# Kernel optimization log

Measured on AMD Instinct MI355X. Metric: run time of the kernel, lower is better.

## Reference

```python
import jax, jax.numpy as jnp
import numpy as np

B, S, D = 4, 2048, 1024  # batch, seq (== context_size), d_in == d_out


def setup_inputs() -> dict:
    key = jax.random.key(0)
    ks = jax.random.split(key, 4)
    scale = 1.0 / np.sqrt(D)
    return {
        "x": jax.random.normal(ks[0], (B, S, D), dtype=jnp.float32),
        "Wq": jax.random.normal(ks[1], (D, D), dtype=jnp.float32) * scale,
        "bq": jnp.zeros((D,), dtype=jnp.float32),
        "Wk": jax.random.normal(ks[2], (D, D), dtype=jnp.float32) * scale,
        "bk": jnp.zeros((D,), dtype=jnp.float32),
        "Wv": jax.random.normal(ks[3], (D, D), dtype=jnp.float32) * scale,
        "bv": jnp.zeros((D,), dtype=jnp.float32),
    }


def reference(x, Wq, bq, Wk, bk, Wv, bv):
    # x: [B, S, D]. Linear layers: y = x @ W^T + b (torch convention: W is [out, in];
    # here W is stored [in, out] already so y = x @ W + b).
    q = jnp.einsum("bsd,df->bsf", x, Wq) + bq
    k = jnp.einsum("bsd,df->bsf", x, Wk) + bk
    v = jnp.einsum("bsd,df->bsf", x, Wv) + bv
    scores = jnp.einsum("bqf,bkf->bqk", q, k)  # [B, S, S]
    causal = jnp.tril(jnp.ones((S, S), dtype=bool))  # mask upper triangle (future)
    scores = jnp.where(causal, scores, -jnp.inf)
    # original divides by sqrt(d_out) after masking
    attn = jax.nn.softmax(scores * (1.0 / jnp.sqrt(jnp.asarray(D, scores.dtype))), axis=-1)
    # dropout rate = 0.0 (identity)
    return jnp.einsum("bqk,bkf->bqf", attn, v)
```

## Files before the change

### kernel.cpp

```cpp
#include <hip/hip_runtime.h>
#include <cstdint>
#include <cstddef>


typedef __attribute__((ext_vector_type(8))) __bf16 bf16x8;
typedef __attribute__((ext_vector_type(4))) float f32x4;
typedef __attribute__((ext_vector_type(4))) float float4v;
typedef __attribute__((ext_vector_type(8))) unsigned short u16x8;
typedef __attribute__((ext_vector_type(4))) unsigned short u16x4;

#define DEVI static __device__ __forceinline__

static constexpr int SS = 2048;
static constexpr int DD = 1024;
static constexpr float SCALE = 0.03125f;

DEVI unsigned short f2bf(float f) {
  unsigned int u = __builtin_bit_cast(unsigned int, f);
  u += 0x7fffu + ((u >> 16) & 1u);
  return (unsigned short)(u >> 16);
}
DEVI float bf2f(unsigned short h) {
  unsigned int u = ((unsigned int)h) << 16;
  return __builtin_bit_cast(float, u);
}

DEVI void gload16(const void* g, void* l) {
  __builtin_amdgcn_global_load_lds(
      (const __attribute__((address_space(1))) unsigned int*)g,
      (__attribute__((address_space(3))) unsigned int*)l, 16, 0, 0);
}

DEVI void gemm_core512(const unsigned short* __restrict__ A,
                       const unsigned short* __restrict__ Bt,
                       int lda, int ldb, int m0, int n0, int K,
                       unsigned short* As, unsigned short* Bs,
                       f32x4 acc[4][2]) {
  const int t = threadIdx.x;
  const int l = t & 63, w = t >> 6;
  const int wr = w >> 2, wc = w & 3;
  const int srow = t >> 2;
  const int scol = (t & 3) * 8;
  const unsigned short* ga = A + (size_t)(m0 + srow) * lda + scol;
  const unsigned short* gb = Bt + (size_t)(n0 + srow) * ldb + scol;
  unsigned short* la = As + t * 8;
  unsigned short* lb = Bs + t * 8;
  const int aoff = (wr * 64 + (l & 15)) * 32 + (l >> 4) * 8;
  const int boff = (wc * 32 + (l & 15)) * 32 + (l >> 4) * 8;
  for (int kk = 0; kk < K; kk += 32) {
    gload16(ga + kk, la);
    gload16(gb + kk, lb);
    __syncthreads();
    bf16x8 av[4], bv[2];
#pragma unroll
    for (int i = 0; i < 4; ++i) av[i] = *(const bf16x8*)(As + aoff + i * 512);
#pragma unroll
    for (int i = 0; i < 2; ++i) bv[i] = *(const bf16x8*)(Bs + boff + i * 512);
#pragma unroll
    for (int mi = 0; mi < 4; ++mi)
#pragma unroll
      for (int ni = 0; ni < 2; ++ni)
        acc[mi][ni] = __builtin_amdgcn_mfma_f32_16x16x32_bf16(
            av[mi], bv[ni], acc[mi][ni], 0, 0, 0);
    __syncthreads();
  }
}

__global__ __launch_bounds__(256) void k_conv_x(const float* __restrict__ x,
                                                unsigned short* __restrict__ xb) {
  size_t i = ((size_t)blockIdx.x * 256 + threadIdx.x) * 4;
  float4v v = *(const float4v*)(x + i);
  u16x4 o;
#pragma unroll
  for (int j = 0; j < 4; ++j) o[j] = f2bf(v[j]);
  *(u16x4*)(xb + i) = o;
}

__global__ __launch_bounds__(256) void k_prep_w(const float* __restrict__ Wq,
                                                const float* __restrict__ Wk,
                                                const float* __restrict__ Wv,
                                                unsigned short* __restrict__ Wt) {
  const int z = blockIdx.z;
  const float* W = (z == 0) ? Wq : (z == 1) ? Wk : Wv;
  unsigned short* O = Wt + (size_t)z * DD * DD;
  const int c0 = blockIdx.x * 64, r0 = blockIdx.y * 64;
  __shared__ unsigned short T[64][72];
  const int t = threadIdx.x;
#pragma unroll
  for (int i = 0; i < 4; ++i) {
    int idx = t + i * 256;
    int row = idx >> 4;
    int c4 = (idx & 15) * 4;
    float4v v = *(const float4v*)(W + (size_t)(r0 + row) * DD + c0 + c4);
#pragma unroll
    for (int j = 0; j < 4; ++j) T[row][c4 + j] = f2bf(v[j]);
  }
  __syncthreads();
#pragma unroll
  for (int i = 0; i < 2; ++i) {
    int idx = t + i * 256;
    int n = idx >> 3;
    int g = (idx & 7) * 8;
    u16x8 u;
#pragma unroll
    for (int j = 0; j < 8; ++j) u[j] = T[g + j][n];
    *(u16x8*)(O + (size_t)(c0 + n) * DD + r0 + g) = u;
  }
}

__global__ __launch_bounds__(512, 4) void k_qk_gemm(
    const unsigned short* __restrict__ xb,
    const unsigned short* __restrict__ Wqt,
    const unsigned short* __restrict__ Wkt,
    const float* __restrict__ bq, const float* __restrict__ bk,
    unsigned short* __restrict__ qb, unsigned short* __restrict__ kb) {
  __shared__ unsigned short As[4096], Bs[4096];
  const int z = blockIdx.z;
  const unsigned short* Bt = z ? Wkt : Wqt;
  const float* bias = z ? bk : bq;
  unsigned short* C = z ? kb : qb;
  const int m0 = blockIdx.x * 128, n0 = blockIdx.y * 128;
  f32x4 acc[4][2];
#pragma unroll
  for (int i = 0; i < 4; ++i)
#pragma unroll
    for (int j = 0; j < 2; ++j) acc[i][j] = f32x4{0.f, 0.f, 0.f, 0.f};
  gemm_core512(xb, Bt, DD, DD, m0, n0, DD, As, Bs, acc);
  const int t = threadIdx.x, l = t & 63, w = t >> 6, wr = w >> 2, wc = w & 3;
  const int fr = (l >> 4) * 4, fc = l & 15;
#pragma unroll
  for (int mi = 0; mi < 4; ++mi)
#pragma unroll
    for (int ni = 0; ni < 2; ++ni) {
      int gc = n0 + wc * 32 + ni * 16 + fc;
      float bv_ = bias[gc];
#pragma unroll
      for (int r = 0; r < 4; ++r) {
        int gr = m0 + wr * 64 + mi * 16 + fr + r;
        C[(size_t)gr * DD + gc] = f2bf(acc[mi][ni][r] + bv_);
      }
    }
}

__global__ __launch_bounds__(512, 4) void k_vt_gemm(
    const unsigned short* __restrict__ Wvt,
    const unsigned short* __restrict__ xb,
    const float* __restrict__ bv, unsigned short* __restrict__ vt) {
  __shared__ unsigned short As[4096], Bs[4096];
  const int b = blockIdx.z;
  const int m0 = blockIdx.x * 128;
  const int n0 = blockIdx.y * 128;
  f32x4 acc[4][2];
#pragma unroll
  for (int i = 0; i < 4; ++i)
#pragma unroll
    for (int j = 0; j < 2; ++j) acc[i][j] = f32x4{0.f, 0.f, 0.f, 0.f};
  gemm_core512(Wvt, xb + (size_t)b * SS * DD, DD, DD, m0, n0, DD, As, Bs, acc);
  unsigned short* C = vt + (size_t)b * DD * SS;
  const int t = threadIdx.x, l = t & 63, w = t >> 6, wr = w >> 2, wc = w & 3;
  const int fr = (l >> 4) * 4, fc = l & 15;
#pragma unroll
  for (int mi = 0; mi < 4; ++mi)
#pragma unroll
    for (int ni = 0; ni < 2; ++ni) {
      int gc = n0 + wc * 32 + ni * 16 + fc;
#pragma unroll
      for (int r = 0; r < 4; ++r) {
        int gr = m0 + wr * 64 + mi * 16 + fr + r;
        C[(size_t)gr * SS + gc] = f2bf(acc[mi][ni][r] + bv[gr]);
      }
    }
}

__global__ __launch_bounds__(512, 4) void k_scores(
    const unsigned short* __restrict__ qb,
    const unsigned short* __restrict__ kb,
    unsigned short* __restrict__ P,
    float* __restrict__ mT, float* __restrict__ lT) {
  const int kt = blockIdx.x, qt = blockIdx.y, b = blockIdx.z;
  if (kt > qt) return;
  __shared__ unsigned short As[4096], Bs[4096];
  __shared__ float redm[4][128];
  __shared__ float redl[4][128];
  f32x4 acc[4][2];
#pragma unroll
  for (int i = 0; i < 4; ++i)
#pragma unroll
    for (int j = 0; j < 2; ++j) acc[i][j] = f32x4{0.f, 0.f, 0.f, 0.f};
  const unsigned short* qp = qb + (size_t)b * SS * DD;
  const unsigned short* kp = kb + (size_t)b * SS * DD;
  gemm_core512(qp, kp, DD, DD, qt * 128, kt * 128, DD, As, Bs, acc);

  const int t = threadIdx.x, l = t & 63, w = t >> 6, wr = w >> 2, wc = w & 3;
  const int fr = (l >> 4) * 4, fc = l & 15;
  const bool diag = (kt == qt);
#pragma unroll
  for (int mi = 0; mi < 4; ++mi)
#pragma unroll
    for (int ni = 0; ni < 2; ++ni) {
      int lc = wc * 32 + ni * 16 + fc;
#pragma unroll
      for (int r = 0; r < 4; ++r) {
        int lr = wr * 64 + mi * 16 + fr + r;
        float s = acc[mi][ni][r] * SCALE;
        if (diag && lc > lr) s = -INFINITY;
        acc[mi][ni][r] = s;
      }
    }
  float rmax[4][4];
#pragma unroll
  for (int mi = 0; mi < 4; ++mi)
#pragma unroll
    for (int r = 0; r < 4; ++r)
      rmax[mi][r] = fmaxf(acc[mi][0][r], acc[mi][1][r]);
#pragma unroll
  for (int d = 1; d < 16; d <<= 1)
#pragma unroll
    for (int mi = 0; mi < 4; ++mi)
#pragma unroll
      for (int r = 0; r < 4; ++r)
        rmax[mi][r] = fmaxf(rmax[mi][r], __shfl_xor(rmax[mi][r], d));
  if ((l & 15) == 0) {
#pragma unroll
    for (int mi = 0; mi < 4; ++mi)
#pragma unroll
      for (int r = 0; r < 4; ++r)
        redm[wc][wr * 64 + mi * 16 + fr + r] = rmax[mi][r];
  }
  __syncthreads();
  float mtv[4][4];
#pragma unroll
  for (int mi = 0; mi < 4; ++mi)
#pragma unroll
    for (int r = 0; r < 4; ++r) {
      int row_l = wr * 64 + mi * 16 + fr + r;
      mtv[mi][r] = fmaxf(fmaxf(redm[0][row_l], redm[1][row_l]),
                         fmaxf(redm[2][row_l], redm[3][row_l]));
    }
  float rsum[4][4];
#pragma unroll
  for (int mi = 0; mi < 4; ++mi)
#pragma unroll
    for (int ni = 0; ni < 2; ++ni)
#pragma unroll
      for (int r = 0; r < 4; ++r) {
        float p = __expf(acc[mi][ni][r] - mtv[mi][r]);
        acc[mi][ni][r] = p;
        if (ni == 0) rsum[mi][r] = p; else rsum[mi][r] += p;
      }
#pragma unroll
  for (int d = 1; d < 16; d <<= 1)
#pragma unroll
    for (int mi = 0; mi < 4; ++mi)
#pragma unroll
      for (int r = 0; r < 4; ++r)
        rsum[mi][r] += __shfl_xor(rsum[mi][r], d);
  if ((l & 15) == 0) {
#pragma unroll
    for (int mi = 0; mi < 4; ++mi)
#pragma unroll
      for (int r = 0; r < 4; ++r)
        redl[wc][wr * 64 + mi * 16 + fr + r] = rsum[mi][r];
  }
  __syncthreads();
  if (wc == 0 && (l & 15) == 0) {
#pragma unroll
    for (int mi = 0; mi < 4; ++mi)
#pragma unroll
      for (int r = 0; r < 4; ++r) {
        int row_l = wr * 64 + mi * 16 + fr + r;
        int gq = qt * 128 + row_l;
        mT[((size_t)b * 16 + kt) * SS + gq] = mtv[mi][r];
        lT[((size_t)b * 16 + kt) * SS + gq] =
            redl[0][row_l] + redl[1][row_l] + redl[2][row_l] + redl[3][row_l];
      }
  }
  unsigned short* Pp = P + (size_t)b * SS * SS;
#pragma unroll
  for (int mi = 0; mi < 4; ++mi)
#pragma unroll
    for (int ni = 0; ni < 2; ++ni) {
      int gc = kt * 128 + wc * 32 + ni * 16 + fc;
#pragma unroll
      for (int r = 0; r < 4; ++r) {
        int gr = qt * 128 + wr * 64 + mi * 16 + fr + r;
        Pp[(size_t)gr * SS + gc] = f2bf(acc[mi][ni][r]);
      }
    }
}

__global__ __launch_bounds__(256) void k_combine(float* __restrict__ mT,
                                                 const float* __restrict__ lT) {
  const int idx = blockIdx.x * 256 + threadIdx.x;
  const int b = idx >> 11, q = idx & 2047;
  const int qt = q >> 7;
  float mv[16];
  float m = -INFINITY;
#pragma unroll
  for (int kt = 0; kt < 16; ++kt)
    if (kt <= qt) {
      mv[kt] = mT[((size_t)b * 16 + kt) * SS + q];
      m = fmaxf(m, mv[kt]);
    }
  float lsum = 0.f;
#pragma unroll
  for (int kt = 0; kt < 16; ++kt)
    if (kt <= qt) lsum += lT[((size_t)b * 16 + kt) * SS + q] * __expf(mv[kt] - m);
  const float inv = 1.f / lsum;
#pragma unroll
  for (int kt = 0; kt < 16; ++kt)
    if (kt <= qt) mT[((size_t)b * 16 + kt) * SS + q] = __expf(mv[kt] - m) * inv;
}

__global__ __launch_bounds__(512, 4) void k_pv(
    const unsigned short* __restrict__ P,
    const unsigned short* __restrict__ vt,
    const float* __restrict__ F, float* __restrict__ out) {
  __shared__ unsigned short As[4096], Bs[4096];
  __shared__ float Flds[2048];
  const int b = blockIdx.z;
  const int n0 = blockIdx.x * 128;
  const int qt = blockIdx.y;
  const int m0 = qt * 128;
  const int nchunk = qt + 1;
  const int t = threadIdx.x, l = t & 63, w = t >> 6, wr = w >> 2, wc = w & 3;
  const int fr = (l >> 4) * 4, fc = l & 15;
  for (int idx = t; idx < nchunk * 128; idx += 512)
    Flds[idx] = F[((size_t)b * 16 + (idx >> 7)) * SS + m0 + (idx & 127)];
  f32x4 accO[4][2], accP[4][2];
#pragma unroll
  for (int i = 0; i < 4; ++i)
#pragma unroll
    for (int j = 0; j < 2; ++j) {
      accO[i][j] = f32x4{0.f, 0.f, 0.f, 0.f};
      accP[i][j] = f32x4{0.f, 0.f, 0.f, 0.f};
    }
  const unsigned short* Pp = P + (size_t)b * SS * SS;
  const unsigned short* Vp = vt + (size_t)b * DD * SS;
  const int srow = t >> 2, scol = (t & 3) * 8;
  const unsigned short* ga = Pp + (size_t)(m0 + srow) * SS + scol;
  const unsigned short* gb = Vp + (size_t)(n0 + srow) * SS + scol;
  unsigned short* la = As + t * 8;
  unsigned short* lb = Bs + t * 8;
  const int aoff = (wr * 64 + (l & 15)) * 32 + (l >> 4) * 8;
  const int boff = (wc * 32 + (l & 15)) * 32 + (l >> 4) * 8;
  for (int c = 0; c < nchunk; ++c) {
#pragma unroll
    for (int s = 0; s < 4; ++s) {
      const int kk = c * 128 + s * 32;
      gload16(ga + kk, la);
      gload16(gb + kk, lb);
      __syncthreads();
      bf16x8 av[4], bv[2];
#pragma unroll
      for (int i = 0; i < 4; ++i) av[i] = *(const bf16x8*)(As + aoff + i * 512);
#pragma unroll
      for (int i = 0; i < 2; ++i) bv[i] = *(const bf16x8*)(Bs + boff + i * 512);
#pragma unroll
      for (int mi = 0; mi < 4; ++mi)
#pragma unroll
        for (int ni = 0; ni < 2; ++ni)
          accP[mi][ni] = __builtin_amdgcn_mfma_f32_16x16x32_bf16(
              av[mi], bv[ni], accP[mi][ni], 0, 0, 0);
      __syncthreads();
    }
#pragma unroll
    for (int mi = 0; mi < 4; ++mi)
#pragma unroll
      for (int r = 0; r < 4; ++r) {
        const float f = Flds[c * 128 + wr * 64 + mi * 16 + fr + r];
#pragma unroll
        for (int ni = 0; ni < 2; ++ni) {
          accO[mi][ni][r] += f * accP[mi][ni][r];
          accP[mi][ni][r] = 0.f;
        }
      }
  }
  float* O = out + (size_t)b * SS * DD;
#pragma unroll
  for (int mi = 0; mi < 4; ++mi)
#pragma unroll
    for (int ni = 0; ni < 2; ++ni) {
      int gc = n0 + wc * 32 + ni * 16 + fc;
#pragma unroll
      for (int r = 0; r < 4; ++r) {
        int gr = m0 + wr * 64 + mi * 16 + fr + r;
        O[(size_t)gr * DD + gc] = accO[mi][ni][r];
      }
    }
}

extern "C" void kernel_launch(void* const* d_in, const int* in_sizes, int n_in,
                              void* d_out, int out_size, void* d_ws, size_t ws_size,
                              hipStream_t stream) {
  (void)in_sizes; (void)n_in; (void)out_size; (void)ws_size;
  const float* x  = (const float*)d_in[0];
  const float* Wq = (const float*)d_in[1];
  const float* bq = (const float*)d_in[2];
  const float* Wk = (const float*)d_in[3];
  const float* bk = (const float*)d_in[4];
  const float* Wv = (const float*)d_in[5];
  const float* bv = (const float*)d_in[6];
  float* out = (float*)d_out;

  char* w = (char*)d_ws;
  unsigned short* xb  = (unsigned short*)(w + 0);
  unsigned short* Wt  = (unsigned short*)(w + 16777216);
  unsigned short* qb  = (unsigned short*)(w + 23068672);
  unsigned short* kb  = (unsigned short*)(w + 39845888);
  unsigned short* vt  = (unsigned short*)(w + 56623104);
  unsigned short* P   = (unsigned short*)(w + 73400320);
  float*          mT  = (float*)(w + 106954752);
  float*          lT  = (float*)(w + 107479040);
  unsigned short* Wqt = Wt;
  unsigned short* Wkt = Wt + (size_t)DD * DD;
  unsigned short* Wvt = Wt + (size_t)2 * DD * DD;

  k_conv_x<<<dim3(8192), dim3(256), 0, stream>>>(x, xb);
  k_prep_w<<<dim3(16, 16, 3), dim3(256), 0, stream>>>(Wq, Wk, Wv, Wt);
  k_qk_gemm<<<dim3(64, 8, 2), dim3(512), 0, stream>>>(xb, Wqt, Wkt, bq, bk, qb, kb);
  k_vt_gemm<<<dim3(8, 16, 4), dim3(512), 0, stream>>>(Wvt, xb, bv, vt);
  k_scores<<<dim3(16, 16, 4), dim3(512), 0, stream>>>(qb, kb, P, mT, lT);
  k_combine<<<dim3(32), dim3(256), 0, stream>>>(mT, lT);
  k_pv<<<dim3(8, 16, 4), dim3(512), 0, stream>>>(P, vt, mT, out);
}
```

Before: 295.5 us.

## Double-buffer LDS tiles in GEMM cores, compact causal grid, reverse PV order

The shared GEMM core now uses two LDS buffers, so the global-to-LDS load for the next K slice is issued before the MFMAs on the current slice, and one barrier per step is removed. The score kernel launches only the 136 lower-triangular tiles per batch, mapping each linear block index to (qt, kt), so no blocks exit early. The PV kernel gets the same double-buffered loop and schedules the heaviest query tiles first to balance load. LDS use per block doubles, which may lower occupancy.

```diff
diff --git a/kernel.cpp b/kernel.cpp
--- a/kernel.cpp
+++ b/kernel.cpp
@@ -31,11 +31,11 @@
       (__attribute__((address_space(3))) unsigned int*)l, 16, 0, 0);
 }
 
-DEVI void gemm_core512(const unsigned short* __restrict__ A,
-                       const unsigned short* __restrict__ Bt,
-                       int lda, int ldb, int m0, int n0, int K,
-                       unsigned short* As, unsigned short* Bs,
-                       f32x4 acc[4][2]) {
+DEVI void gemm2ph(const unsigned short* __restrict__ A,
+                  const unsigned short* __restrict__ Bt,
+                  int lda, int ldb, int m0, int n0, int K,
+                  unsigned short* As, unsigned short* Bs,
+                  f32x4 acc[4][2]) {
   const int t = threadIdx.x;
   const int l = t & 63, w = t >> 6;
   const int wr = w >> 2, wc = w & 3;
@@ -47,15 +47,24 @@
   unsigned short* lb = Bs + t * 8;
   const int aoff = (wr * 64 + (l & 15)) * 32 + (l >> 4) * 8;
   const int boff = (wc * 32 + (l & 15)) * 32 + (l >> 4) * 8;
-  for (int kk = 0; kk < K; kk += 32) {
-    gload16(ga + kk, la);
-    gload16(gb + kk, lb);
-    __syncthreads();
+  const int nt = K >> 5;
+  gload16(ga, la);
+  gload16(gb, lb);
+  __syncthreads();
+  int cur = 0;
+  for (int ti = 0; ti < nt; ++ti) {
+    if (ti + 1 < nt) {
+      const int kk = (ti + 1) << 5;
+      gload16(ga + kk, la + (cur ^ 1) * 4096);
+      gload16(gb + kk, lb + (cur ^ 1) * 4096);
+    }
+    const unsigned short* Ab = As + cur * 4096;
+    const unsigned short* Bb = Bs + cur * 4096;
     bf16x8 av[4], bv[2];
 #pragma unroll
-    for (int i = 0; i < 4; ++i) av[i] = *(const bf16x8*)(As + aoff + i * 512);
-#pragma unroll
-    for (int i = 0; i < 2; ++i) bv[i] = *(const bf16x8*)(Bs + boff + i * 512);
+    for (int i = 0; i < 4; ++i) av[i] = *(const bf16x8*)(Ab + aoff + i * 512);
+#pragma unroll
+    for (int i = 0; i < 2; ++i) bv[i] = *(const bf16x8*)(Bb + boff + i * 512);
 #pragma unroll
     for (int mi = 0; mi < 4; ++mi)
 #pragma unroll
@@ -63,6 +72,7 @@
         acc[mi][ni] = __builtin_amdgcn_mfma_f32_16x16x32_bf16(
             av[mi], bv[ni], acc[mi][ni], 0, 0, 0);
     __syncthreads();
+    cur ^= 1;
   }
 }
 
@@ -114,7 +124,7 @@
     const unsigned short* __restrict__ Wkt,
     const float* __restrict__ bq, const float* __restrict__ bk,
     unsigned short* __restrict__ qb, unsigned short* __restrict__ kb) {
-  __shared__ unsigned short As[4096], Bs[4096];
+  __shared__ unsigned short As[8192], Bs[8192];
   const int z = blockIdx.z;
   const unsigned short* Bt = z ? Wkt : Wqt;
   const float* bias = z ? bk : bq;
@@ -125,7 +135,7 @@
   for (int i = 0; i < 4; ++i)
 #pragma unroll
     for (int j = 0; j < 2; ++j) acc[i][j] = f32x4{0.f, 0.f, 0.f, 0.f};
-  gemm_core512(xb, Bt, DD, DD, m0, n0, DD, As, Bs, acc);
+  gemm2ph(xb, Bt, DD, DD, m0, n0, DD, As, Bs, acc);
   const int t = threadIdx.x, l = t & 63, w = t >> 6, wr = w >> 2, wc = w & 3;
   const int fr = (l >> 4) * 4, fc = l & 15;
 #pragma unroll
@@ -146,7 +156,7 @@
     const unsigned short* __restrict__ Wvt,
     const unsigned short* __restrict__ xb,
     const float* __restrict__ bv, unsigned short* __restrict__ vt) {
-  __shared__ unsigned short As[4096], Bs[4096];
+  __shared__ unsigned short As[8192], Bs[8192];
   const int b = blockIdx.z;
   const int m0 = blockIdx.x * 128;
   const int n0 = blockIdx.y * 128;
@@ -155,7 +165,7 @@
   for (int i = 0; i < 4; ++i)
 #pragma unroll
     for (int j = 0; j < 2; ++j) acc[i][j] = f32x4{0.f, 0.f, 0.f, 0.f};
-  gemm_core512(Wvt, xb + (size_t)b * SS * DD, DD, DD, m0, n0, DD, As, Bs, acc);
+  gemm2ph(Wvt, xb + (size_t)b * SS * DD, DD, DD, m0, n0, DD, As, Bs, acc);
   unsigned short* C = vt + (size_t)b * DD * SS;
   const int t = threadIdx.x, l = t & 63, w = t >> 6, wr = w >> 2, wc = w & 3;
   const int fr = (l >> 4) * 4, fc = l & 15;
@@ -177,9 +187,12 @@
     const unsigned short* __restrict__ kb,
     unsigned short* __restrict__ P,
     float* __restrict__ mT, float* __restrict__ lT) {
-  const int kt = blockIdx.x, qt = blockIdx.y, b = blockIdx.z;
-  if (kt > qt) return;
-  __shared__ unsigned short As[4096], Bs[4096];
+  const int p = blockIdx.x, b = blockIdx.z;
+  int qt = (int)((sqrtf(8.f * (float)p + 1.f) - 1.f) * 0.5f);
+  while ((qt + 1) * (qt + 2) / 2 <= p) ++qt;
+  while (qt * (qt + 1) / 2 > p) --qt;
+  const int kt = p - qt * (qt + 1) / 2;
+  __shared__ unsigned short As[8192], Bs[8192];
   __shared__ float redm[4][128];
   __shared__ float redl[4][128];
   f32x4 acc[4][2];
@@ -189,7 +202,7 @@
     for (int j = 0; j < 2; ++j) acc[i][j] = f32x4{0.f, 0.f, 0.f, 0.f};
   const unsigned short* qp = qb + (size_t)b * SS * DD;
   const unsigned short* kp = kb + (size_t)b * SS * DD;
-  gemm_core512(qp, kp, DD, DD, qt * 128, kt * 128, DD, As, Bs, acc);
+  gemm2ph(qp, kp, DD, DD, qt * 128, kt * 128, DD, As, Bs, acc);
 
   const int t = threadIdx.x, l = t & 63, w = t >> 6, wr = w >> 2, wc = w & 3;
   const int fr = (l >> 4) * 4, fc = l & 15;
@@ -244,9 +257,9 @@
     for (int ni = 0; ni < 2; ++ni)
 #pragma unroll
       for (int r = 0; r < 4; ++r) {
-        float p = __expf(acc[mi][ni][r] - mtv[mi][r]);
-        acc[mi][ni][r] = p;
-        if (ni == 0) rsum[mi][r] = p; else rsum[mi][r] += p;
+        float pv = __expf(acc[mi][ni][r] - mtv[mi][r]);
+        acc[mi][ni][r] = pv;
+        if (ni == 0) rsum[mi][r] = pv; else rsum[mi][r] += pv;
       }
 #pragma unroll
   for (int d = 1; d < 16; d <<= 1)
@@ -316,16 +329,16 @@
     const unsigned short* __restrict__ P,
     const unsigned short* __restrict__ vt,
     const float* __restrict__ F, float* __restrict__ out) {
-  __shared__ unsigned short As[4096], Bs[4096];
+  __shared__ unsigned short As[8192], Bs[8192];
   __shared__ float Flds[2048];
   const int b = blockIdx.z;
   const int n0 = blockIdx.x * 128;
-  const int qt = blockIdx.y;
+  const int qt = 15 - blockIdx.y;
   const int m0 = qt * 128;
-  const int nchunk = qt + 1;
+  const int nsteps = (qt + 1) * 4;
   const int t = threadIdx.x, l = t & 63, w = t >> 6, wr = w >> 2, wc = w & 3;
   const int fr = (l >> 4) * 4, fc = l & 15;
-  for (int idx = t; idx < nchunk * 128; idx += 512)
+  for (int idx = t; idx < (qt + 1) * 128; idx += 512)
     Flds[idx] = F[((size_t)b * 16 + (idx >> 7)) * SS + m0 + (idx & 127)];
   f32x4 accO[4][2], accP[4][2];
 #pragma unroll
@@ -344,37 +357,45 @@
   unsigned short* lb = Bs + t * 8;
   const int aoff = (wr * 64 + (l & 15)) * 32 + (l >> 4) * 8;
   const int boff = (wc * 32 + (l & 15)) * 32 + (l >> 4) * 8;
-  for (int c = 0; c < nchunk; ++c) {
-#pragma unroll
-    for (int s = 0; s < 4; ++s) {
-      const int kk = c * 128 + s * 32;
-      gload16(ga + kk, la);
-      gload16(gb + kk, lb);
-      __syncthreads();
-      bf16x8 av[4], bv[2];
-#pragma unroll
-      for (int i = 0; i < 4; ++i) av[i] = *(const bf16x8*)(As + aoff + i * 512);
-#pragma unroll
-      for (int i = 0; i < 2; ++i) bv[i] = *(const bf16x8*)(Bs + boff + i * 512);
+  gload16(ga, la);
+  gload16(gb, lb);
+  __syncthreads();
+  int cur = 0;
+  for (int i = 0; i < nsteps; ++i) {
+    if (i + 1 < nsteps) {
+      const int kk = (i + 1) << 5;
+      gload16(ga + kk, la + (cur ^ 1) * 4096);
+      gload16(gb + kk, lb + (cur ^ 1) * 4096);
+    }
+    const unsigned short* Ab = As + cur * 4096;
+    const unsigned short* Bb = Bs + cur * 4096;
+    bf16x8 av[4], bv[2];
+#pragma unroll
+    for (int ii = 0; ii < 4; ++ii) av[ii] = *(const bf16x8*)(Ab + aoff + ii * 512);
+#pragma unroll
+    for (int ii = 0; ii < 2; ++ii) bv[ii] = *(const bf16x8*)(Bb + boff + ii * 512);
+#pragma unroll
+    for (int mi = 0; mi < 4; ++mi)
+#pragma unroll
+      for (int ni = 0; ni < 2; ++ni)
+        accP[mi][ni] = __builtin_amdgcn_mfma_f32_16x16x32_bf16(
+            av[mi], bv[ni], accP[mi][ni], 0, 0, 0);
+    if ((i & 3) == 3) {
+      const int c = i >> 2;
 #pragma unroll
       for (int mi = 0; mi < 4; ++mi)
 #pragma unroll
-        for (int ni = 0; ni < 2; ++ni)
-          accP[mi][ni] = __builtin_amdgcn_mfma_f32_16x16x32_bf16(
-              av[mi], bv[ni], accP[mi][ni], 0, 0, 0);
-      __syncthreads();
-    }
-#pragma unroll
-    for (int mi = 0; mi < 4; ++mi)
-#pragma unroll
-      for (int r = 0; r < 4; ++r) {
-        const float f = Flds[c * 128 + wr * 64 + mi * 16 + fr + r];
-#pragma unroll
-        for (int ni = 0; ni < 2; ++ni) {
-          accO[mi][ni][r] += f * accP[mi][ni][r];
-          accP[mi][ni][r] = 0.f;
+        for (int r = 0; r < 4; ++r) {
+          const float f = Flds[c * 128 + wr * 64 + mi * 16 + fr + r];
+#pragma unroll
+          for (int ni = 0; ni < 2; ++ni) {
+            accO[mi][ni][r] += f * accP[mi][ni][r];
+            accP[mi][ni][r] = 0.f;
+          }
         }
-      }
+    }
+    __syncthreads();
+    cur ^= 1;
   }
   float* O = out + (size_t)b * SS * DD;
 #pragma unroll
@@ -420,7 +441,7 @@
   k_prep_w<<<dim3(16, 16, 3), dim3(256), 0, stream>>>(Wq, Wk, Wv, Wt);
   k_qk_gemm<<<dim3(64, 8, 2), dim3(512), 0, stream>>>(xb, Wqt, Wkt, bq, bk, qb, kb);
   k_vt_gemm<<<dim3(8, 16, 4), dim3(512), 0, stream>>>(Wvt, xb, bv, vt);
-  k_scores<<<dim3(16, 16, 4), dim3(512), 0, stream>>>(qb, kb, P, mT, lT);
+  k_scores<<<dim3(136, 1, 4), dim3(512), 0, stream>>>(qb, kb, P, mT, lT);
   k_combine<<<dim3(32), dim3(256), 0, stream>>>(mT, lT);
   k_pv<<<dim3(8, 16, 4), dim3(512), 0, stream>>>(P, vt, mT, out);
 }
```

Result: no change. 297.9 us (+0.8%).
